# Performance work log

Measured on AMD Instinct MI355X. Metric: run time of the kernel, lower is better.

The kernel has to match this reference:

```python
import jax, jax.numpy as jnp
import numpy as np

D_MODEL = 1024
D_STATE = 32
K = 4
B_SZ = 2
L_SEQ = 1024
DT_MIN = 0.001
DT_MAX = 0.2


def setup_inputs() -> dict:
    key = jax.random.key(0)
    ks = jax.random.split(key, 10)
    n = lambda k, s: jax.random.normal(k, s, dtype=jnp.float32)
    D, N = D_MODEL, D_STATE
    return {
        "x": n(ks[0], (B_SZ, L_SEQ, D)),
        "W_in": 0.02 * n(ks[1], (D, 2 * D)),
        "b_in": jnp.zeros((2 * D,), jnp.float32),
        "conv_w": 0.2 * n(ks[2], (D, 1, K)),   # depthwise conv kernel (O,I/g,K)
        "conv_b": jnp.zeros((D,), jnp.float32),
        "A_log": -2.0 + 0.1 * n(ks[3], (D, N)),
        "wB": 0.02 * n(ks[4], (D, N)),
        "bB": jnp.zeros((D, N), jnp.float32),
        "wC": 0.02 * n(ks[5], (D, N)),
        "bC": jnp.zeros((D, N), jnp.float32),
        "W_dt": 0.02 * n(ks[6], (D, D)),
        "b_dt": jnp.zeros((D,), jnp.float32),
        "W_out": 0.02 * n(ks[7], (D, D)),
        "b_out": jnp.zeros((D,), jnp.float32),
        "ln_g": jnp.ones((D,), jnp.float32),
        "ln_b": jnp.zeros((D,), jnp.float32),
    }


def reference(x, W_in, b_in, conv_w, conv_b, A_log, wB, bB, wC, bC,
              W_dt, b_dt, W_out, b_out, ln_g, ln_b):
    Bsz, L, D = x.shape
    N = A_log.shape[1]
    residual = x
    # input projection -> x path and gate z
    xz = x @ W_in + b_in
    xp, z = jnp.split(xz, 2, axis=-1)
    # causal depthwise conv1d (left-pad k-1)
    xt = jnp.swapaxes(xp, 1, 2)  # (B, D, L)
    y = jax.lax.conv_general_dilated(
        xt, conv_w, window_strides=(1,), padding=[(K - 1, 0)],
        dimension_numbers=("NCH", "OIH", "NCH"), feature_group_count=D)
    x_conv = jnp.swapaxes(y + conv_b[None, :, None], 1, 2)  # (B, L, D)
    xs = jax.nn.silu(x_conv)
    # selective SSM parameters
    A = -jnp.exp(jnp.clip(A_log, -5.0, 2.0))          # (D, N)
    Bt = xs[..., None] * wB + bB                      # (B, L, D, N) grouped 1x1 conv
    Ct = xs[..., None] * wC + bC                      # (B, L, D, N)
    dt = jnp.clip(jax.nn.softplus(xs @ W_dt + b_dt), DT_MIN, DT_MAX)  # (B, L, D)

    def step(states, inp):
        dt_i, B_i, C_i, x_i = inp  # (B,D), (B,D,N), (B,D,N), (B,D)
        A_bar = jnp.exp(jnp.clip(dt_i[..., None] * A, -10.0, 0.0))
        st = jnp.clip(states * A_bar + dt_i[..., None] * B_i * x_i[..., None],
                      -10.0, 10.0)
        return st, jnp.sum(C_i * st, axis=-1)

    states0 = jnp.zeros((Bsz, D, N), x.dtype)
    tl = lambda a: jnp.moveaxis(a, 1, 0)  # time-leading for scan
    _, ys = jax.lax.scan(step, states0, (tl(dt), tl(Bt), tl(Ct), tl(xs)))
    scan_out = jnp.moveaxis(ys, 0, 1) * jax.nn.silu(z)  # (B, L, D)
    out = scan_out @ W_out + b_out
    h = out + residual
    mu = jnp.mean(h, axis=-1, keepdims=True)
    var = jnp.var(h, axis=-1, keepdims=True)
    return (h - mu) / jnp.sqrt(var + 1e-5) * ln_g + ln_b
```

## Files before the change

kernel.cpp:

```cpp
#include <hip/hip_runtime.h>
#include <hip/hip_bf16.h>
#include <math.h>

#define D_MODEL 1024
#define D_STATE 32
#define LSEQ    1024
#define BSZ     2
#define MROWS   (BSZ*LSEQ)
#define NSEG    16
#define SEGL    (LSEQ/NSEG)
#define SCD     8
#define LOG2E   1.4426950408889634f

typedef unsigned short u16;
typedef unsigned int   u32;
typedef __bf16 bf16x8 __attribute__((ext_vector_type(8)));
typedef float  f32x4  __attribute__((ext_vector_type(4)));

__device__ __forceinline__ u16 f2b(float v) {
    unsigned int b = __float_as_uint(v);
    return (u16)((b + 0x7FFFu + ((b >> 16) & 1u)) >> 16);
}
__device__ __forceinline__ float b2f(u16 v) {
    return __uint_as_float((unsigned)v << 16);
}
__device__ __forceinline__ float softplus_clip(float v) {
    float sp = fmaxf(v, 0.f) + log1pf(__expf(-fabsf(v)));
    return fminf(fmaxf(sp, 0.001f), 0.2f);
}
__device__ __forceinline__ float silu(float v) {
    return v / (1.f + __expf(-v));
}

#define GLOAD16(g, l) __builtin_amdgcn_global_load_lds(                     \
    (__attribute__((address_space(1))) void*)(g),                           \
    (__attribute__((address_space(3))) void*)(l), 16, 0, 0)

__global__ __launch_bounds__(256)
void cvt_k(const float* __restrict__ in, u16* __restrict__ out) {
    int i = blockIdx.x * 256 + threadIdx.x;
    float4 v = ((const float4*)in)[i];
    ushort4 o;
    o.x = f2b(v.x); o.y = f2b(v.y); o.z = f2b(v.z); o.w = f2b(v.w);
    ((ushort4*)out)[i] = o;
}

__global__ __launch_bounds__(256)
void tcvt_k(const float* __restrict__ W, u16* __restrict__ Wt, int K, int N) {
    __shared__ u16 tile[32][33];
    const int n0 = blockIdx.x * 32, k0 = blockIdx.y * 32;
    const int tx = threadIdx.x & 31, ty = threadIdx.x >> 5;
#pragma unroll
    for (int r = 0; r < 32; r += 8)
        tile[r + ty][tx] = f2b(W[(size_t)(k0 + r + ty) * N + n0 + tx]);
    __syncthreads();
#pragma unroll
    for (int r = 0; r < 32; r += 8)
        Wt[(size_t)(n0 + r + ty) * K + k0 + tx] = tile[tx][r + ty];
}

template<int EPI, int OD>
__global__ __launch_bounds__(256)
void mgemm2_k(const u16* __restrict__ A, const u16* __restrict__ Bt,
              const float* __restrict__ bias, const float* __restrict__ res,
              void* __restrict__ Cv, int M, int N, int K) {
    __shared__ u16 As[2][4096];
    __shared__ u16 Bs[2][4096];
    const int t  = threadIdx.x;
    const int l  = t & 63;
    const int w  = t >> 6;
    const int wr = w >> 1, wc = w & 1;
    const int fr = l & 15, fq = l >> 4;

    const int nx  = N >> 6;
    const int nwg = (M >> 6) * nx;
    int wg = blockIdx.y * nx + blockIdx.x;
    int sw = (wg & 7) * (nwg >> 3) + (wg >> 3);
    const int bm = (sw / nx) << 6;
    const int bn = (sw % nx) << 6;

    const int srow = t >> 3;
    const int scol = ((t & 7) * 8) ^ ((srow & 7) << 3);
    const u16* Ap0 = A  + (size_t)(bm + srow)      * K + scol;
    const u16* Ap1 = A  + (size_t)(bm + 32 + srow) * K + scol;
    const u16* Bp0 = Bt + (size_t)(bn + srow)      * K + scol;
    const u16* Bp1 = Bt + (size_t)(bn + 32 + srow) * K + scol;

    f32x4 acc[2][2] = {};

#define STAGE2(buf, k0)                                      \
    GLOAD16(Ap0 + (k0), &As[buf][t * 8]);                    \
    GLOAD16(Ap1 + (k0), &As[buf][2048 + t * 8]);             \
    GLOAD16(Bp0 + (k0), &Bs[buf][t * 8]);                    \
    GLOAD16(Bp1 + (k0), &Bs[buf][2048 + t * 8]);

    STAGE2(0, 0)
    asm volatile("s_waitcnt vmcnt(0)" ::: "memory");
    __syncthreads();

    const int NT = K >> 6;
    int cur = 0;
    for (int ks = 0; ks < NT; ++ks) {
        if (ks + 1 < NT) { STAGE2(cur ^ 1, (ks + 1) << 6) }
        bf16x8 af[2][2], bf[2][2];
#pragma unroll
        for (int m = 0; m < 2; ++m) {
            const int r = wr * 32 + m * 16 + fr;
            const int xo = (r & 7) << 3;
#pragma unroll
            for (int kk = 0; kk < 2; ++kk)
                af[m][kk] = *(const bf16x8*)&As[cur][r * 64 + ((kk * 32 + fq * 8) ^ xo)];
        }
#pragma unroll
        for (int n = 0; n < 2; ++n) {
            const int c = wc * 32 + n * 16 + fr;
            const int xo = (c & 7) << 3;
#pragma unroll
            for (int kk = 0; kk < 2; ++kk)
                bf[n][kk] = *(const bf16x8*)&Bs[cur][c * 64 + ((kk * 32 + fq * 8) ^ xo)];
        }
#pragma unroll
        for (int m = 0; m < 2; ++m)
#pragma unroll
            for (int n = 0; n < 2; ++n)
#pragma unroll
                for (int kk = 0; kk < 2; ++kk)
                    acc[m][n] = __builtin_amdgcn_mfma_f32_16x16x32_bf16(
                        af[m][kk], bf[n][kk], acc[m][n], 0, 0, 0);
        asm volatile("s_waitcnt vmcnt(0)" ::: "memory");
        __syncthreads();
        cur ^= 1;
    }
#undef STAGE2

#pragma unroll
    for (int m = 0; m < 2; ++m) {
        const int row = bm + wr * 32 + m * 16 + fq * 4;
#pragma unroll
        for (int n = 0; n < 2; ++n) {
            const int col = bn + wc * 32 + n * 16 + fr;
            float bi = (EPI == 3) ? 0.f : bias[col];
#pragma unroll
            for (int j = 0; j < 4; ++j) {
                float v = acc[m][n][j];
                if (EPI == 3) v = softplus_clip(v + bias[row + j]);
                else          v += bi;
                if (EPI == 2) v += res[(size_t)(row + j) * N + col];
                if (OD == 1) ((u16*)Cv)[(size_t)(row + j) * N + col] = f2b(v);
                else         ((float*)Cv)[(size_t)(row + j) * N + col] = v;
            }
        }
    }
}

__global__ __launch_bounds__(256)
void convT_k(const u16* __restrict__ xz, const float* __restrict__ cw,
             const float* __restrict__ cb,
             u16* __restrict__ xsb, u16* __restrict__ xsT,
             u16* __restrict__ zsT) {
    const int l0 = blockIdx.x * 64;
    const int d0 = blockIdx.y * 64;
    const int b  = blockIdx.z;
    const int t  = threadIdx.x;
    __shared__ float xin[67][68];
    __shared__ float xo[64][69];
    const int lr = t >> 4, c4 = (t & 15) << 2;
    const u16* srcx = xz + ((size_t)b * LSEQ + l0 - 3) * 2048 + d0;
#pragma unroll
    for (int p = 0; p < 5; ++p) {
        int r = p * 16 + lr;
        if (r < 67) {
            float4 v = make_float4(0.f, 0.f, 0.f, 0.f);
            if (l0 + r >= 3) {
                ushort4 u = *(const ushort4*)(srcx + (size_t)r * 2048 + c4);
                v = make_float4(b2f(u.x), b2f(u.y), b2f(u.z), b2f(u.w));
            }
            *(float4*)&xin[r][c4] = v;
        }
    }
    __syncthreads();
    const int dd = t & 63;
    const int wv = t >> 6;
    float4 w4 = *(const float4*)(cw + ((size_t)(d0 + dd)) * 4);
    float cbv = cb[d0 + dd];
    float win[19];
#pragma unroll
    for (int i = 0; i < 19; ++i) win[i] = xin[wv * 16 + i][dd];
    u16* xrow = xsb + ((size_t)b * LSEQ + l0 + wv * 16) * D_MODEL + d0 + dd;
#pragma unroll
    for (int i = 0; i < 16; ++i) {
        float a = cbv;
        a = fmaf(win[i],     w4.x, a);
        a = fmaf(win[i + 1], w4.y, a);
        a = fmaf(win[i + 2], w4.z, a);
        a = fmaf(win[i + 3], w4.w, a);
        float r = silu(a);
        xrow[(size_t)i * D_MODEL] = f2b(r);
        xo[dd][wv * 16 + i] = r;
    }
    __syncthreads();
    {
        const int dr = t >> 2, ls = (t & 3) << 4;
        u16* dst = xsT + ((size_t)(d0 + dr)) * MROWS + (size_t)b * LSEQ + l0 + ls;
        ushort4 o[4];
#pragma unroll
        for (int j = 0; j < 16; ++j)
            ((u16*)o)[j] = f2b(xo[dr][ls + j]);
#pragma unroll
        for (int j = 0; j < 4; ++j)
            ((ushort4*)dst)[j] = o[j];
    }
    __syncthreads();
    const u16* srcz = xz + ((size_t)b * LSEQ + l0) * 2048 + 1024 + d0;
#pragma unroll
    for (int p = 0; p < 4; ++p) {
        int r = p * 16 + lr;
        ushort4 u = *(const ushort4*)(srcz + (size_t)r * 2048 + c4);
        xo[c4 + 0][r] = silu(b2f(u.x));
        xo[c4 + 1][r] = silu(b2f(u.y));
        xo[c4 + 2][r] = silu(b2f(u.z));
        xo[c4 + 3][r] = silu(b2f(u.w));
    }
    __syncthreads();
    {
        const int dr = t >> 2, ls = (t & 3) << 4;
        u16* dst = zsT + ((size_t)(d0 + dr)) * MROWS + (size_t)b * LSEQ + l0 + ls;
        ushort4 o[4];
#pragma unroll
        for (int j = 0; j < 16; ++j)
            ((u16*)o)[j] = f2b(xo[dr][ls + j]);
#pragma unroll
        for (int j = 0; j < 4; ++j)
            ((ushort4*)dst)[j] = o[j];
    }
}

__global__ __launch_bounds__(256, 4)
void scan_a(const u16* __restrict__ xsT, const u16* __restrict__ dtT,
            const float* __restrict__ A_log, const float* __restrict__ wB,
            const float* __restrict__ bB,
            float* __restrict__ Qbuf, float* __restrict__ sdtb) {
    const int t   = threadIdx.x;
    const int grp = t >> 5, g = t & 31;
    const int d   = blockIdx.x * SCD + grp;
    const int seg = blockIdx.y, b = blockIdx.z;
    const size_t chb = (size_t)d * MROWS + (size_t)b * LSEQ + (size_t)seg * SEGL;
    const int pi  = d * D_STATE + g;

    const float A2  = -__expf(fminf(fmaxf(A_log[pi], -5.f), 2.f)) * LOG2E;
    const float wB0 = wB[pi], bB0 = bB[pi];
    float s = 0.f, sdt = 0.f;

    for (int l0 = 0; l0 < SEGL; l0 += 32) {
        u16 xu = xsT[chb + l0 + g];
        u16 du = dtT[chb + l0 + g];
        sdt += b2f(du);
        u32 pk = ((u32)xu << 16) | du;
#pragma unroll
        for (int h = 0; h < 2; ++h) {
            float av[16], dbv[16];
#pragma unroll
            for (int u = 0; u < 16; ++u) {
                u32 p = (u32)__shfl((int)pk, h * 16 + u, 32);
                float xa = __uint_as_float(p & 0xffff0000u);
                float da = __uint_as_float(p << 16);
                av[u]  = __builtin_amdgcn_exp2f(da * A2);
                dbv[u] = (da * xa) * fmaf(xa, wB0, bB0);
            }
#pragma unroll
            for (int u = 0; u < 16; ++u)
                s = fmaf(s, av[u], dbv[u]);
        }
    }
    sdt += __shfl_xor(sdt, 1);
    sdt += __shfl_xor(sdt, 2);
    sdt += __shfl_xor(sdt, 4);
    sdt += __shfl_xor(sdt, 8);
    sdt += __shfl_xor(sdt, 16);
    const size_t qb = ((size_t)b * D_MODEL + d) * NSEG + seg;
    Qbuf[qb * 32 + g] = s;
    if (g == 0) sdtb[qb] = sdt;
}

__global__ __launch_bounds__(256, 4)
void scan_c(const u16* __restrict__ xsT, const u16* __restrict__ dtT,
            const u16* __restrict__ zsT,
            const float* __restrict__ A_log, const float* __restrict__ wB,
            const float* __restrict__ bB, const float* __restrict__ wC,
            const float* __restrict__ bC,
            const float* __restrict__ Qbuf, const float* __restrict__ sdtb,
            u16* __restrict__ so) {
    const int t   = threadIdx.x;
    const int grp = t >> 5, g = t & 31;
    const int d   = blockIdx.x * SCD + grp;
    const int seg = blockIdx.y, b = blockIdx.z;
    const size_t chb = (size_t)d * MROWS + (size_t)b * LSEQ + (size_t)seg * SEGL;
    const int pi  = d * D_STATE + g;

    const float A2  = -__expf(fminf(fmaxf(A_log[pi], -5.f), 2.f)) * LOG2E;
    const float wB0 = wB[pi], bB0 = bB[pi];
    const float wC0 = wC[pi], bC0 = bC[pi];

    float s = 0.f;
    const size_t qb = ((size_t)b * D_MODEL + d) * NSEG;
    for (int j = 0; j < seg; ++j) {
        float qj = Qbuf[(qb + j) * 32 + g];
        float pj = __builtin_amdgcn_exp2f(A2 * sdtb[qb + j]);
        s = fmaf(s, pj, qj);
    }

    __shared__ u16 tile[32][10];
    const size_t obase = ((size_t)b * LSEQ + (size_t)seg * SEGL) * D_MODEL
                       + blockIdx.x * SCD;

    for (int l0 = 0; l0 < SEGL; l0 += 32) {
        u16 xu = xsT[chb + l0 + g];
        u16 du = dtT[chb + l0 + g];
        float zw = b2f(zsT[chb + l0 + g]);
        u32 pk = ((u32)xu << 16) | du;
        float w_[32];
#pragma unroll
        for (int h = 0; h < 2; ++h) {
            float av[16], dbv[16], cv[16];
#pragma unroll
            for (int u = 0; u < 16; ++u) {
                u32 p = (u32)__shfl((int)pk, h * 16 + u, 32);
                float xa = __uint_as_float(p & 0xffff0000u);
                float da = __uint_as_float(p << 16);
                av[u]  = __builtin_amdgcn_exp2f(da * A2);
                dbv[u] = (da * xa) * fmaf(xa, wB0, bB0);
                cv[u]  = fmaf(xa, wC0, bC0);
            }
#pragma unroll
            for (int u = 0; u < 16; ++u) {
                s = fmaf(s, av[u], dbv[u]);
                w_[h * 16 + u] = cv[u] * s;
            }
        }
#pragma unroll
        for (int u = 0; u < 16; ++u) {
            float snd = (g & 16) ? w_[u] : w_[u + 16];
            float rcv = __shfl_xor(snd, 16);
            w_[u] = ((g & 16) ? w_[u + 16] : w_[u]) + rcv;
        }
#pragma unroll
        for (int u = 0; u < 8; ++u) {
            float snd = (g & 8) ? w_[u] : w_[u + 8];
            float rcv = __shfl_xor(snd, 8);
            w_[u] = ((g & 8) ? w_[u + 8] : w_[u]) + rcv;
        }
#pragma unroll
        for (int u = 0; u < 4; ++u) {
            float snd = (g & 4) ? w_[u] : w_[u + 4];
            float rcv = __shfl_xor(snd, 4);
            w_[u] = ((g & 4) ? w_[u + 4] : w_[u]) + rcv;
        }
#pragma unroll
        for (int u = 0; u < 2; ++u) {
            float snd = (g & 2) ? w_[u] : w_[u + 2];
            float rcv = __shfl_xor(snd, 2);
            w_[u] = ((g & 2) ? w_[u + 2] : w_[u]) + rcv;
        }
        {
            float snd = (g & 1) ? w_[0] : w_[1];
            float rcv = __shfl_xor(snd, 1);
            w_[0] = ((g & 1) ? w_[1] : w_[0]) + rcv;
        }
        float sv = w_[0] * zw;
        __syncthreads();
        tile[g][grp] = f2b(sv);
        __syncthreads();
        {
            int i = t >> 3, j = t & 7;
            so[obase + (size_t)(l0 + i) * D_MODEL + j] = tile[i][j];
        }
    }
}

__global__ __launch_bounds__(256)
void ln_k(const float* __restrict__ h, const float* __restrict__ gam,
          const float* __restrict__ bet, float* __restrict__ out) {
    int row = blockIdx.x;
    const float* hr = h + (size_t)row * D_MODEL;
    int t = threadIdx.x;
    float4 v = *(const float4*)(hr + (t << 2));
    float s  = v.x + v.y + v.z + v.w;
    float ss = v.x * v.x + v.y * v.y + v.z * v.z + v.w * v.w;
#pragma unroll
    for (int m = 1; m < 64; m <<= 1) {
        s  += __shfl_xor(s,  m, 64);
        ss += __shfl_xor(ss, m, 64);
    }
    __shared__ float red[8];
    int wid = t >> 6, lane = t & 63;
    if (lane == 0) { red[wid] = s; red[4 + wid] = ss; }
    __syncthreads();
    s  = red[0] + red[1] + red[2] + red[3];
    ss = red[4] + red[5] + red[6] + red[7];
    float mu  = s * (1.f / D_MODEL);
    float var = ss * (1.f / D_MODEL) - mu * mu;
    float r = rsqrtf(var + 1e-5f);
    float4 g4 = *(const float4*)(gam + (t << 2));
    float4 b4 = *(const float4*)(bet + (t << 2));
    float4 o;
    o.x = (v.x - mu) * r * g4.x + b4.x;
    o.y = (v.y - mu) * r * g4.y + b4.y;
    o.z = (v.z - mu) * r * g4.z + b4.z;
    o.w = (v.w - mu) * r * g4.w + b4.w;
    *(float4*)(out + (size_t)row * D_MODEL + (t << 2)) = o;
}

extern "C" void kernel_launch(void* const* d_in, const int* in_sizes, int n_in,
                              void* d_out, int out_size, void* d_ws, size_t ws_size,
                              hipStream_t stream) {
    const float* x      = (const float*)d_in[0];
    const float* W_in   = (const float*)d_in[1];
    const float* b_in   = (const float*)d_in[2];
    const float* conv_w = (const float*)d_in[3];
    const float* conv_b = (const float*)d_in[4];
    const float* A_log  = (const float*)d_in[5];
    const float* wB     = (const float*)d_in[6];
    const float* bB     = (const float*)d_in[7];
    const float* wC     = (const float*)d_in[8];
    const float* bC     = (const float*)d_in[9];
    const float* W_dt   = (const float*)d_in[10];
    const float* b_dt   = (const float*)d_in[11];
    const float* W_out  = (const float*)d_in[12];
    const float* b_out  = (const float*)d_in[13];
    const float* ln_g   = (const float*)d_in[14];
    const float* ln_b   = (const float*)d_in[15];
    float* out = (float*)d_out;

    const size_t MB = 1024 * 1024;
    char* w = (char*)d_ws;
    u16*   xz    = (u16*)  (w);
    u16*   xsT   = (u16*)  (w + 8  * MB);
    u16*   zsT   = (u16*)  (w + 12 * MB);
    u16*   xsb16 = (u16*)  (w + 16 * MB);
    u16*   xb    = (u16*)  (w + 20 * MB);
    u16*   WinT  = (u16*)  (w + 24 * MB);
    u16*   WdtT  = (u16*)  (w + 28 * MB);
    u16*   WoutT = (u16*)  (w + 30 * MB);
    u16*   dtT   = (u16*)  (w + 32 * MB);
    float* Qbuf  = (float*)(w + 36 * MB);
    float* sdtb  = (float*)(w + 40 * MB);
    float* hb    = (float*)(w);
    u16*   sob16 = xb;

    dim3 blk(256);
    cvt_k<<<dim3(MROWS * D_MODEL / 1024), blk, 0, stream>>>(x, xb);
    tcvt_k<<<dim3(2048 / 32, D_MODEL / 32), blk, 0, stream>>>(W_in,  WinT,  D_MODEL, 2048);
    tcvt_k<<<dim3(D_MODEL / 32, D_MODEL / 32), blk, 0, stream>>>(W_dt,  WdtT,  D_MODEL, D_MODEL);
    tcvt_k<<<dim3(D_MODEL / 32, D_MODEL / 32), blk, 0, stream>>>(W_out, WoutT, D_MODEL, D_MODEL);

    mgemm2_k<0, 1><<<dim3(2048 / 64, MROWS / 64), blk, 0, stream>>>(
        xb, WinT, b_in, nullptr, xz, MROWS, 2048, D_MODEL);
    convT_k<<<dim3(LSEQ / 64, D_MODEL / 64, BSZ), blk, 0, stream>>>(
        xz, conv_w, conv_b, xsb16, xsT, zsT);
    mgemm2_k<3, 1><<<dim3(MROWS / 64, D_MODEL / 64), blk, 0, stream>>>(
        WdtT, xsb16, b_dt, nullptr, dtT, D_MODEL, MROWS, D_MODEL);
    scan_a<<<dim3(D_MODEL / SCD, NSEG, BSZ), blk, 0, stream>>>(
        xsT, dtT, A_log, wB, bB, Qbuf, sdtb);
    scan_c<<<dim3(D_MODEL / SCD, NSEG, BSZ), blk, 0, stream>>>(
        xsT, dtT, zsT, A_log, wB, bB, wC, bC, Qbuf, sdtb, sob16);
    mgemm2_k<2, 0><<<dim3(D_MODEL / 64, MROWS / 64), blk, 0, stream>>>(
        sob16, WoutT, b_out, x, hb, MROWS, D_MODEL, D_MODEL);
    ln_k<<<dim3(MROWS), blk, 0, stream>>>(hb, ln_g, ln_b, out);
}
```

Before: 123.7 us.

## Double scan segment count and merge weight/input conversion kernels into one launch

Raises the number of scan segments from 16 to 32 so each segment is a single 32-step chunk, which doubles scan block count and shortens the serial recurrence per block, at the cost of a longer serial prefix over segment summaries in scan_c. Separately, the input conversion and three weight transpose-convert kernels are fused into one launch indexed by a flat job id, removing three kernel launches. The sdt buffer offset is moved so the larger Qbuf does not overlap it.

```diff
diff --git a/kernel.cpp b/kernel.cpp
--- a/kernel.cpp
+++ b/kernel.cpp
@@ -7,7 +7,7 @@
 #define LSEQ    1024
 #define BSZ     2
 #define MROWS   (BSZ*LSEQ)
-#define NSEG    16
+#define NSEG    32
 #define SEGL    (LSEQ/NSEG)
 #define SCD     8
 #define LOG2E   1.4426950408889634f
@@ -37,18 +37,27 @@
     (__attribute__((address_space(3))) void*)(l), 16, 0, 0)
 
 __global__ __launch_bounds__(256)
-void cvt_k(const float* __restrict__ in, u16* __restrict__ out) {
-    int i = blockIdx.x * 256 + threadIdx.x;
-    float4 v = ((const float4*)in)[i];
-    ushort4 o;
-    o.x = f2b(v.x); o.y = f2b(v.y); o.z = f2b(v.z); o.w = f2b(v.w);
-    ((ushort4*)out)[i] = o;
-}
-
-__global__ __launch_bounds__(256)
-void tcvt_k(const float* __restrict__ W, u16* __restrict__ Wt, int K, int N) {
+void wprep_k(const float* __restrict__ W_in, const float* __restrict__ W_dt,
+             const float* __restrict__ W_out, const float* __restrict__ x,
+             u16* __restrict__ WinT, u16* __restrict__ WdtT,
+             u16* __restrict__ WoutT, u16* __restrict__ xb) {
+    int job = blockIdx.x;
+    if (job >= 4096) {
+        int i = (job - 4096) * 256 + threadIdx.x;
+        float4 v = ((const float4*)x)[i];
+        ushort4 o;
+        o.x = f2b(v.x); o.y = f2b(v.y); o.z = f2b(v.z); o.w = f2b(v.w);
+        ((ushort4*)xb)[i] = o;
+        return;
+    }
+    const float* W; u16* Wt; int N;
+    if (job < 2048)      { W = W_in;  Wt = WinT;  N = 2048; }
+    else if (job < 3072) { W = W_dt;  Wt = WdtT;  N = 1024; job -= 2048; }
+    else                 { W = W_out; Wt = WoutT; N = 1024; job -= 3072; }
+    const int K = 1024;
+    const int ntx = N >> 5;
+    const int n0 = (job % ntx) << 5, k0 = (job / ntx) << 5;
     __shared__ u16 tile[32][33];
-    const int n0 = blockIdx.x * 32, k0 = blockIdx.y * 32;
     const int tx = threadIdx.x & 31, ty = threadIdx.x >> 5;
 #pragma unroll
     for (int r = 0; r < 32; r += 8)
@@ -249,28 +258,26 @@
 
     const float A2  = -__expf(fminf(fmaxf(A_log[pi], -5.f), 2.f)) * LOG2E;
     const float wB0 = wB[pi], bB0 = bB[pi];
-    float s = 0.f, sdt = 0.f;
-
-    for (int l0 = 0; l0 < SEGL; l0 += 32) {
-        u16 xu = xsT[chb + l0 + g];
-        u16 du = dtT[chb + l0 + g];
-        sdt += b2f(du);
-        u32 pk = ((u32)xu << 16) | du;
-#pragma unroll
-        for (int h = 0; h < 2; ++h) {
-            float av[16], dbv[16];
-#pragma unroll
-            for (int u = 0; u < 16; ++u) {
-                u32 p = (u32)__shfl((int)pk, h * 16 + u, 32);
-                float xa = __uint_as_float(p & 0xffff0000u);
-                float da = __uint_as_float(p << 16);
-                av[u]  = __builtin_amdgcn_exp2f(da * A2);
-                dbv[u] = (da * xa) * fmaf(xa, wB0, bB0);
-            }
-#pragma unroll
-            for (int u = 0; u < 16; ++u)
-                s = fmaf(s, av[u], dbv[u]);
-        }
+    float s = 0.f;
+
+    u16 xu = xsT[chb + g];
+    u16 du = dtT[chb + g];
+    float sdt = b2f(du);
+    u32 pk = ((u32)xu << 16) | du;
+#pragma unroll
+    for (int h = 0; h < 2; ++h) {
+        float av[16], dbv[16];
+#pragma unroll
+        for (int u = 0; u < 16; ++u) {
+            u32 p = (u32)__shfl((int)pk, h * 16 + u, 32);
+            float xa = __uint_as_float(p & 0xffff0000u);
+            float da = __uint_as_float(p << 16);
+            av[u]  = __builtin_amdgcn_exp2f(da * A2);
+            dbv[u] = (da * xa) * fmaf(xa, wB0, bB0);
+        }
+#pragma unroll
+        for (int u = 0; u < 16; ++u)
+            s = fmaf(s, av[u], dbv[u]);
     }
     sdt += __shfl_xor(sdt, 1);
     sdt += __shfl_xor(sdt, 2);
@@ -313,10 +320,10 @@
     const size_t obase = ((size_t)b * LSEQ + (size_t)seg * SEGL) * D_MODEL
                        + blockIdx.x * SCD;
 
-    for (int l0 = 0; l0 < SEGL; l0 += 32) {
-        u16 xu = xsT[chb + l0 + g];
-        u16 du = dtT[chb + l0 + g];
-        float zw = b2f(zsT[chb + l0 + g]);
+    {
+        u16 xu = xsT[chb + g];
+        u16 du = dtT[chb + g];
+        float zw = b2f(zsT[chb + g]);
         u32 pk = ((u32)xu << 16) | du;
         float w_[32];
 #pragma unroll
@@ -372,7 +379,7 @@
         __syncthreads();
         {
             int i = t >> 3, j = t & 7;
-            so[obase + (size_t)(l0 + i) * D_MODEL + j] = tile[i][j];
+            so[obase + (size_t)i * D_MODEL + j] = tile[i][j];
         }
     }
 }
@@ -443,15 +450,13 @@
     u16*   WoutT = (u16*)  (w + 30 * MB);
     u16*   dtT   = (u16*)  (w + 32 * MB);
     float* Qbuf  = (float*)(w + 36 * MB);
-    float* sdtb  = (float*)(w + 40 * MB);
+    float* sdtb  = (float*)(w + 44 * MB);
     float* hb    = (float*)(w);
     u16*   sob16 = xb;
 
     dim3 blk(256);
-    cvt_k<<<dim3(MROWS * D_MODEL / 1024), blk, 0, stream>>>(x, xb);
-    tcvt_k<<<dim3(2048 / 32, D_MODEL / 32), blk, 0, stream>>>(W_in,  WinT,  D_MODEL, 2048);
-    tcvt_k<<<dim3(D_MODEL / 32, D_MODEL / 32), blk, 0, stream>>>(W_dt,  WdtT,  D_MODEL, D_MODEL);
-    tcvt_k<<<dim3(D_MODEL / 32, D_MODEL / 32), blk, 0, stream>>>(W_out, WoutT, D_MODEL, D_MODEL);
+    wprep_k<<<dim3(6144), blk, 0, stream>>>(W_in, W_dt, W_out, x,
+                                            WinT, WdtT, WoutT, xb);
 
     mgemm2_k<0, 1><<<dim3(2048 / 64, MROWS / 64), blk, 0, stream>>>(
         xb, WinT, b_in, nullptr, xz, MROWS, 2048, D_MODEL);
```

Result: no change. 126.2 us (+2.0%).
